# Kernel tuning notes

Hardware: AMD Instinct MI355X
Metric: run time of the kernel (lower is better)

Reference implementation:

```python
import jax, jax.numpy as jnp
import numpy as np

# dims: batch, seq, model dim, heads, head_k_dim, head_v_dim, conv size
B, S, D, H, DK, DV, K = 1, 2048, 1024, 8, 128, 128, 4
KD, VD = H * DK, H * DV  # key_dim, value_dim


def _silu(x):
    return x * jax.nn.sigmoid(x)


def _l2norm(x, eps=1e-6):
    return x * jax.lax.rsqrt(jnp.sum(x * x, -1, keepdims=True) + eps)


def _causal_conv_silu(x, w):
    # depthwise causal conv1d (ShortConvolution, activation='silu', no bias)
    # x: [b, s, d], w: [d, K]
    Kc = w.shape[1]
    xp = jnp.pad(x, ((0, 0), (Kc - 1, 0), (0, 0)))
    y = sum(xp[:, i:i + x.shape[1], :] * w[:, i] for i in range(Kc))
    return _silu(y)


def _rmsnorm(x, w, eps=1e-5):
    return x * jax.lax.rsqrt(jnp.mean(x * x, -1, keepdims=True) + eps) * w


def _kda(q, k, v, g, beta):
    # gated delta-rule linear attention (KDA), recurrent form == chunk_kda math
    # q,k,g: [B,S,H,DK]; v: [B,S,H,DV]; beta: [B,S,H]
    scale = DK ** -0.5
    qn = _l2norm(q) * scale  # use_qk_l2norm_in_kernel=True
    kn = _l2norm(k)

    def step(Sm, inp):
        q_t, k_t, v_t, g_t, b_t = inp  # [B,H,DK], [B,H,DK], [B,H,DV], [B,H,DK], [B,H]
        Sm = Sm * jnp.exp(g_t)[..., None]                    # per-key-channel decay
        v_new = (v_t - jnp.einsum('bhk,bhkv->bhv', k_t, Sm)) * b_t[..., None]
        Sm = Sm + k_t[..., None] * v_new[..., None, :]       # delta-rule update
        o_t = jnp.einsum('bhk,bhkv->bhv', q_t, Sm)
        return Sm, o_t

    xs = (jnp.swapaxes(qn, 0, 1), jnp.swapaxes(kn, 0, 1), jnp.swapaxes(v, 0, 1),
          jnp.swapaxes(g, 0, 1), jnp.swapaxes(beta, 0, 1))
    S0 = jnp.zeros((q.shape[0], H, DK, DV), jnp.float32)
    _, o = jax.lax.scan(step, S0, xs)
    return jnp.swapaxes(o, 0, 1)  # [B,S,H,DV]


def setup_inputs() -> dict:
    key = jax.random.key(0)
    ks = jax.random.split(key, 20)

    def w(k, shape, fan_in):
        return jax.random.normal(k, shape, jnp.float32) / np.sqrt(fan_in)

    return {
        'x': jax.random.normal(ks[0], (B, S, D), jnp.float32),
        've': jax.random.normal(ks[1], (B, S, D), jnp.float32),
        'sa_lambdas': jax.random.uniform(ks[2], (2,), jnp.float32),
        'Wq': w(ks[3], (KD, D), D), 'Wk': w(ks[4], (KD, D), D), 'Wv': w(ks[5], (VD, D), D),
        'Wo': w(ks[6], (D, VD), VD),
        'wq_conv': w(ks[7], (KD, K), K), 'wk_conv': w(ks[8], (KD, K), K), 'wv_conv': w(ks[9], (VD, K), K),
        'Wf1': w(ks[10], (DV, D), D), 'Wf2': w(ks[11], (KD, DV), DV),
        'Wb': w(ks[12], (H, D), D),
        'A_log': jnp.log(jax.random.uniform(ks[13], (H,), jnp.float32, 1.0, 16.0)),
        'dt_bias': jnp.zeros((KD,), jnp.float32),
        'Wg1': w(ks[14], (DV, D), D), 'Wg2': w(ks[15], (VD, DV), DV),
        'bg2': jnp.zeros((VD,), jnp.float32),
        'w_norm': jnp.ones((DV,), jnp.float32),
    }


def reference(x, ve, sa_lambdas, Wq, Wk, Wv, Wo, wq_conv, wk_conv, wv_conv,
              Wf1, Wf2, Wb, A_log, dt_bias, Wg1, Wg2, bg2, w_norm):
    b, s, _ = x.shape
    # q/k/v projections + short causal conv with silu
    q = _causal_conv_silu(x @ Wq.T, wq_conv)
    k = _causal_conv_silu(x @ Wk.T, wk_conv)
    v = _causal_conv_silu(x @ Wv.T, wv_conv)
    # fused_kda_gate: g = -exp(A_log) * softplus(f_proj(x) + dt_bias), per [H, DK]
    g = (x @ Wf1.T) @ Wf2.T
    g = jax.nn.softplus((g + dt_bias).astype(jnp.float32)).reshape(b, s, H, DK)
    g = -jnp.exp(A_log)[None, None, :, None] * g
    beta = jax.nn.sigmoid((x @ Wb.T).astype(jnp.float32))  # [b,s,H]
    q = q.reshape(b, s, H, DK)
    k = k.reshape(b, s, H, DK)
    v = v.reshape(b, s, H, DV)
    # mix v with value-embedding ve (3-D branch of _mix_v_with_ve)
    ve_v = _causal_conv_silu(ve @ Wv.T, wv_conv).reshape(b, s, H, DV)
    v = sa_lambdas[0] * v + sa_lambdas[1] * ve_v
    o = _kda(q, k, v, g, beta)  # [b,s,H,DV]
    # FusedRMSNormGated(activation='sigmoid'): rmsnorm(o)*w then gate
    g_out = ((x @ Wg1.T) @ Wg2.T + bg2).reshape(b, s, H, DV)
    o = _rmsnorm(o, w_norm) * jax.nn.sigmoid(g_out)
    return o.reshape(b, s, VD) @ Wo.T
```

## Files before the change

### kernel.cpp

```cpp
#include <hip/hip_runtime.h>
#include <math.h>
#include <stdint.h>

#define S_LEN 2048
#define DMODEL 1024
#define NH 8
#define DK_ 128
#define DV_ 128
#define KD_ 1024
#define KCONV 4
#define CW 32
#define NW2 64
#define PREB_STRIDE 17408
#define TKH_OFF 0
#define QHT_OFF 4096
#define KCT_OFF 8192
#define TV_OFF 12288
#define NN_OFF 16384
#define RS 164
#define GS 20

typedef short bf16x8 __attribute__((ext_vector_type(8)));
typedef float f32x4 __attribute__((ext_vector_type(4)));

__device__ __forceinline__ uint16_t f2bf(float f) {
  uint32_t u = __float_as_uint(f);
  u += 0x7FFF + ((u >> 16) & 1);
  return (uint16_t)(u >> 16);
}
__device__ __forceinline__ float bf2f(uint16_t u) {
  return __uint_as_float((uint32_t)u << 16);
}
__device__ __forceinline__ void glds16(const uint16_t* g, uint16_t* l) {
  __builtin_amdgcn_global_load_lds(
      (const __attribute__((address_space(1))) void*)g,
      (__attribute__((address_space(3))) void*)l, 16, 0, 0);
}
__device__ __forceinline__ float dot4(float4 a, float4 b) {
  return fmaf(a.w, b.w, fmaf(a.z, b.z, fmaf(a.y, b.y, a.x * b.x)));
}
__device__ __forceinline__ float4 f4add(float4 a, float4 b) {
  float4 r; r.x = a.x + b.x; r.y = a.y + b.y; r.z = a.z + b.z; r.w = a.w + b.w; return r;
}
__device__ __forceinline__ float4 f4sub(float4 a, float4 b) {
  float4 r; r.x = a.x - b.x; r.y = a.y - b.y; r.z = a.z - b.z; r.w = a.w - b.w; return r;
}
__device__ __forceinline__ float4 f4mul(float4 a, float4 b) {
  float4 r; r.x = a.x * b.x; r.y = a.y * b.y; r.z = a.z * b.z; r.w = a.w * b.w; return r;
}
__device__ __forceinline__ float4 f4s(float4 a, float s) {
  float4 r; r.x = a.x * s; r.y = a.y * s; r.z = a.z * s; r.w = a.w * s; return r;
}
__device__ __forceinline__ float4 f4expc(float4 a) {
  float4 r;
  r.x = expf(fminf(a.x, 0.f)); r.y = expf(fminf(a.y, 0.f));
  r.z = expf(fminf(a.z, 0.f)); r.w = expf(fminf(a.w, 0.f));
  return r;
}
__device__ __forceinline__ float4 f4exp(float4 a) {
  float4 r; r.x = expf(a.x); r.y = expf(a.y); r.z = expf(a.z); r.w = expf(a.w); return r;
}
__device__ __forceinline__ uint4 pack8(float4 a, float4 b) {
  uint4 r;
  r.x = (uint32_t)f2bf(a.x) | ((uint32_t)f2bf(a.y) << 16);
  r.y = (uint32_t)f2bf(a.z) | ((uint32_t)f2bf(a.w) << 16);
  r.z = (uint32_t)f2bf(b.x) | ((uint32_t)f2bf(b.y) << 16);
  r.w = (uint32_t)f2bf(b.z) | ((uint32_t)f2bf(b.w) << 16);
  return r;
}
__device__ __forceinline__ uint2 pack4(f32x4 a) {
  uint2 r;
  r.x = (uint32_t)f2bf(a[0]) | ((uint32_t)f2bf(a[1]) << 16);
  r.y = (uint32_t)f2bf(a[2]) | ((uint32_t)f2bf(a[3]) << 16);
  return r;
}
union U4B8 { uint4 u; bf16x8 b; };
__device__ __forceinline__ bf16x8 u2b(uint4 u) { U4B8 x; x.u = u; return x.b; }

#define DPPADD(x, ctrl) \
  x += __int_as_float(__builtin_amdgcn_update_dpp(0, __float_as_int(x), ctrl, 0xF, 0xF, true))

__device__ __forceinline__ void row8_sum2(float& a, float& b) {
  DPPADD(a, 0xB1); DPPADD(b, 0xB1);
  DPPADD(a, 0x4E); DPPADD(b, 0x4E);
  DPPADD(a, 0x141); DPPADD(b, 0x141);
}
__device__ __forceinline__ void row8_arr8x2(float* x, float* y) {
#pragma unroll
  for (int i = 0; i < 8; i++) { DPPADD(x[i], 0xB1); DPPADD(y[i], 0xB1); }
#pragma unroll
  for (int i = 0; i < 8; i++) { DPPADD(x[i], 0x4E); DPPADD(y[i], 0x4E); }
#pragma unroll
  for (int i = 0; i < 8; i++) { DPPADD(x[i], 0x141); DPPADD(y[i], 0x141); }
}

struct CastArgs {
  const float* s[8];
  uint16_t* d[8];
  int n[8];
};
__global__ __launch_bounds__(256) void cast_multi(CastArgs a, const float* __restrict__ Wb,
                                                  uint16_t* __restrict__ Wbp) {
  int i = blockIdx.y;
  if (i == 8) {
    for (int idx = blockIdx.x * 256 + threadIdx.x; idx < 128 * 1024; idx += 256 * 256) {
      int r = idx >> 10;
      Wbp[idx] = (r < 8) ? f2bf(Wb[idx]) : (uint16_t)0;
    }
    return;
  }
  const int step = gridDim.x * 256 * 8;
  for (int base = (blockIdx.x * 256 + threadIdx.x) * 8; base < a.n[i]; base += step) {
    const float4* sp = (const float4*)(a.s[i] + base);
    float4 x0 = sp[0], x1 = sp[1];
    *(uint4*)(a.d[i] + base) = pack8(x0, x1);
  }
}

__global__ __launch_bounds__(256) void gemm_wc(
    const float* __restrict__ A,
    const float* __restrict__ B,
    uint16_t* __restrict__ C) {
  __shared__ float As[16][68];
  __shared__ float Bs[16][68];
  const int tid = threadIdx.x;
  const int m0 = blockIdx.y * 64, n0 = blockIdx.x * 64;
  const int tx = tid & 15, ty = tid >> 4;
  const int lk = tid & 15, lr = tid >> 4;
  const int bc = tid & 63, bkr = tid >> 6;
  float acc[4][4] = {};
  for (int k0 = 0; k0 < 128; k0 += 16) {
#pragma unroll
    for (int i = 0; i < 4; i++) {
      As[lk][lr + 16 * i] = A[(size_t)(m0 + lr + 16 * i) * 128 + k0 + lk];
      Bs[bkr + 4 * i][bc] = B[(size_t)(k0 + bkr + 4 * i) * 1024 + n0 + bc];
    }
    __syncthreads();
#pragma unroll
    for (int kk = 0; kk < 16; kk++) {
      float4 a4 = *(const float4*)&As[kk][ty * 4];
      float4 b4 = *(const float4*)&Bs[kk][tx * 4];
      float av[4] = {a4.x, a4.y, a4.z, a4.w};
      float bv[4] = {b4.x, b4.y, b4.z, b4.w};
#pragma unroll
      for (int i = 0; i < 4; i++)
#pragma unroll
        for (int jx = 0; jx < 4; jx++) acc[i][jx] = fmaf(av[i], bv[jx], acc[i][jx]);
    }
    __syncthreads();
  }
#pragma unroll
  for (int i = 0; i < 4; i++)
#pragma unroll
    for (int jx = 0; jx < 4; jx++)
      C[(size_t)(m0 + ty * 4 + i) * 1024 + n0 + tx * 4 + jx] = f2bf(acc[i][jx]);
}

__device__ __forceinline__ void gemm_body(
    const uint16_t* __restrict__ A, const uint16_t* __restrict__ B, void* C,
    int N, int K, int outbf, int bx, int by, int tid,
    uint16_t* Asb, uint16_t* Bsb) {
  const int n0 = bx * 128;
  if (n0 >= N) return;
  const int w = tid >> 6, lane = tid & 63;
  const int m0 = by * 128;
  const int mw = (w & 1) * 64, nw = (w >> 1) * 64;
  const int c0 = tid, c1 = 256 + tid;
  const int r0 = c0 >> 2, cl0 = (c0 & 3) ^ ((r0 >> 2) & 3);
  const int r1 = c1 >> 2, cl1 = (c1 & 3) ^ ((r1 >> 2) & 3);
  const uint16_t* gA0 = A + (size_t)(m0 + r0) * K + cl0 * 8;
  const uint16_t* gA1 = A + (size_t)(m0 + r1) * K + cl1 * 8;
  const uint16_t* gB0 = B + (size_t)(n0 + r0) * K + cl0 * 8;
  const uint16_t* gB1 = B + (size_t)(n0 + r1) * K + cl1 * 8;
  uint16_t* lA0 = Asb + w * 512;
  uint16_t* lA1 = Asb + 2048 + w * 512;
  uint16_t* lB0 = Bsb + w * 512;
  uint16_t* lB1 = Bsb + 2048 + w * 512;

  const int l15 = lane & 15, q = lane >> 4;
  const int ccq = q ^ ((l15 >> 2) & 3);

  f32x4 acc[4][4] = {};
  for (int k0 = 0; k0 < K; k0 += 32) {
    glds16(gA0 + k0, lA0);
    glds16(gA1 + k0, lA1);
    glds16(gB0 + k0, lB0);
    glds16(gB1 + k0, lB1);
    __syncthreads();
    bf16x8 af[4], bfr[4];
#pragma unroll
    for (int i = 0; i < 4; i++)
      af[i] = *(const bf16x8*)&Asb[(mw + i * 16 + l15) * 32 + ccq * 8];
#pragma unroll
    for (int jx = 0; jx < 4; jx++)
      bfr[jx] = *(const bf16x8*)&Bsb[(nw + jx * 16 + l15) * 32 + ccq * 8];
#pragma unroll
    for (int i = 0; i < 4; i++)
#pragma unroll
      for (int jx = 0; jx < 4; jx++)
        acc[i][jx] = __builtin_amdgcn_mfma_f32_16x16x32_bf16(af[i], bfr[jx],
                                                             acc[i][jx], 0, 0, 0);
    __syncthreads();
  }
#pragma unroll
  for (int i = 0; i < 4; i++) {
#pragma unroll
    for (int jx = 0; jx < 4; jx++) {
      int n = n0 + nw + jx * 16 + l15;
#pragma unroll
      for (int r = 0; r < 4; r++) {
        int m = m0 + mw + i * 16 + q * 4 + r;
        if (outbf)
          ((uint16_t*)C)[(size_t)m * N + n] = f2bf(acc[i][jx][r]);
        else
          ((float*)C)[(size_t)m * N + n] = acc[i][jx][r];
      }
    }
  }
}

struct GJobs {
  const uint16_t* A[8];
  const uint16_t* B[8];
  void* C[8];
  int N[8];
  int outbf[8];
};
__global__ __launch_bounds__(256) void gemm_mfma(GJobs j, int K) {
  __shared__ uint16_t Asb[128 * 32];
  __shared__ uint16_t Bsb[128 * 32];
  const int z = blockIdx.z;
  gemm_body(j.A[z], j.B[z], j.C[z], j.N[z], K, j.outbf[z],
            blockIdx.x, blockIdx.y, threadIdx.x, Asb, Bsb);
}

__global__ __launch_bounds__(256) void conv_silu_mix(
    const uint16_t* __restrict__ qp, const uint16_t* __restrict__ kp,
    const uint16_t* __restrict__ vp, const uint16_t* __restrict__ vep,
    const float* __restrict__ wq, const float* __restrict__ wk,
    const float* __restrict__ wv, const float* __restrict__ lam,
    float* __restrict__ qc, float* __restrict__ kc, float* __restrict__ vmx) {
  int idx = blockIdx.x * 256 + threadIdx.x;
  if (idx >= S_LEN * KD_ / 8) return;
  int s = idx >> 7;
  int d0 = (idx & 127) * 8;
  const float lam0 = lam[0], lam1 = lam[1];

  union { uint4 u; ushort h[8]; } t;
  size_t base = (size_t)s * KD_ + d0;

  {
    float4 w4[8];
#pragma unroll
    for (int c = 0; c < 8; c++) w4[c] = *(const float4*)(wq + (size_t)d0 * 4 + c * 4);
    float acc[8] = {};
#pragma unroll
    for (int i = 0; i < KCONV; i++) {
      int ss = s - (KCONV - 1) + i;
      if (ss < 0) continue;
      t.u = *(const uint4*)(qp + (size_t)ss * KD_ + d0);
      float wi[8] = {w4[0].x, w4[1].x, w4[2].x, w4[3].x, w4[4].x, w4[5].x, w4[6].x, w4[7].x};
      if (i == 1) { for (int c = 0; c < 8; c++) wi[c] = ((const float*)&w4[c])[1]; }
      if (i == 2) { for (int c = 0; c < 8; c++) wi[c] = ((const float*)&w4[c])[2]; }
      if (i == 3) { for (int c = 0; c < 8; c++) wi[c] = ((const float*)&w4[c])[3]; }
#pragma unroll
      for (int c = 0; c < 8; c++) acc[c] = fmaf(bf2f(t.h[c]), wi[c], acc[c]);
    }
    float out[8];
#pragma unroll
    for (int c = 0; c < 8; c++) out[c] = acc[c] / (1.f + expf(-acc[c]));
    *(float4*)(qc + base) = *(float4*)&out[0];
    *(float4*)(qc + base + 4) = *(float4*)&out[4];
  }
  {
    float4 w4[8];
#pragma unroll
    for (int c = 0; c < 8; c++) w4[c] = *(const float4*)(wk + (size_t)d0 * 4 + c * 4);
    float acc[8] = {};
#pragma unroll
    for (int i = 0; i < KCONV; i++) {
      int ss = s - (KCONV - 1) + i;
      if (ss < 0) continue;
      t.u = *(const uint4*)(kp + (size_t)ss * KD_ + d0);
#pragma unroll
      for (int c = 0; c < 8; c++)
        acc[c] = fmaf(bf2f(t.h[c]), ((const float*)&w4[c])[i], acc[c]);
    }
    float out[8];
#pragma unroll
    for (int c = 0; c < 8; c++) out[c] = acc[c] / (1.f + expf(-acc[c]));
    *(float4*)(kc + base) = *(float4*)&out[0];
    *(float4*)(kc + base + 4) = *(float4*)&out[4];
  }
  {
    float4 w4[8];
#pragma unroll
    for (int c = 0; c < 8; c++) w4[c] = *(const float4*)(wv + (size_t)d0 * 4 + c * 4);
    float av[8] = {}, ae[8] = {};
#pragma unroll
    for (int i = 0; i < KCONV; i++) {
      int ss = s - (KCONV - 1) + i;
      if (ss < 0) continue;
      size_t off = (size_t)ss * KD_ + d0;
      t.u = *(const uint4*)(vp + off);
#pragma unroll
      for (int c = 0; c < 8; c++)
        av[c] = fmaf(bf2f(t.h[c]), ((const float*)&w4[c])[i], av[c]);
      t.u = *(const uint4*)(vep + off);
#pragma unroll
      for (int c = 0; c < 8; c++)
        ae[c] = fmaf(bf2f(t.h[c]), ((const float*)&w4[c])[i], ae[c]);
    }
    float out[8];
#pragma unroll
    for (int c = 0; c < 8; c++) {
      float sv = av[c] / (1.f + expf(-av[c]));
      float se = ae[c] / (1.f + expf(-ae[c]));
      out[c] = lam0 * sv + lam1 * se;
    }
    *(float4*)(vmx + base) = *(float4*)&out[0];
    *(float4*)(vmx + base + 4) = *(float4*)&out[4];
  }
}

__global__ __launch_bounds__(256) void kda_pre(
    const float* __restrict__ qc, const float* __restrict__ kc,
    const float* __restrict__ graw, const float* __restrict__ vm,
    const float* __restrict__ bpre, const float* __restrict__ dt_bias,
    const float* __restrict__ A_log, uint16_t* __restrict__ preB,
    float* __restrict__ preF) {
  __shared__ float kls[32 * RS];
  __shared__ float Gls[32 * RS];
  __shared__ float Mcm[32 * 36];
  __shared__ float bls[32];
  const int w = blockIdx.x >> 3, h = blockIdx.x & 7;
  const int tid = threadIdx.x;
  const int t = tid >> 3, kq = tid & 7;
  const int wv = tid >> 6;
  const size_t gb = (size_t)blockIdx.x * PREB_STRIDE;
  const size_t gf = (size_t)blockIdx.x * 128;

  size_t roff = (size_t)(w * CW + t) * KD_ + h * DK_ + kq * 16;
  float4 kv[4], qv[4], gv[4], dtb[4];
#pragma unroll
  for (int i = 0; i < 4; i++) {
    kv[i] = *(const float4*)(kc + roff + i * 4);
    qv[i] = *(const float4*)(qc + roff + i * 4);
    gv[i] = *(const float4*)(graw + roff + i * 4);
    dtb[i] = *(const float4*)(dt_bias + h * DK_ + kq * 16 + i * 4);
  }
  const float Ahead = expf(A_log[h]);
  if (tid < 32) {
    float b = bpre[(size_t)(w * CW + tid) * 128 + h];
    bls[tid] = 1.f / (1.f + expf(-b));
  }
  float src[32];
  if (tid >= 128) {
    int c2 = tid - 128;
#pragma unroll
    for (int t2 = 0; t2 < 32; t2++)
      src[t2] = vm[(size_t)(w * CW + t2) * KD_ + h * DV_ + c2];
  }
#pragma unroll
  for (int i = 0; i < 4; i++) {
    float vsp[4];
    float xin[4] = {gv[i].x + dtb[i].x, gv[i].y + dtb[i].y,
                    gv[i].z + dtb[i].z, gv[i].w + dtb[i].w};
#pragma unroll
    for (int e = 0; e < 4; e++)
      vsp[e] = (xin[e] > 20.f) ? xin[e] : log1pf(expf(xin[e]));
    gv[i].x = -Ahead * vsp[0]; gv[i].y = -Ahead * vsp[1];
    gv[i].z = -Ahead * vsp[2]; gv[i].w = -Ahead * vsp[3];
  }
  float sk = 0.f, sq = 0.f;
#pragma unroll
  for (int i = 0; i < 4; i++) {
    sk += dot4(kv[i], kv[i]);
    sq += dot4(qv[i], qv[i]);
  }
  row8_sum2(sk, sq);
  float rkn = rsqrtf(sk + 1e-6f);
  float rqn = rsqrtf(sq + 1e-6f) * 0.08838834764831845f;
#pragma unroll
  for (int i = 0; i < 4; i++) {
    kv[i] = f4s(kv[i], rkn);
    qv[i] = f4s(qv[i], rqn);
    *(float4*)&kls[t * RS + kq * GS + i * 4] = kv[i];
    *(float4*)&Gls[t * RS + kq * GS + i * 4] = gv[i];
  }
  __syncthreads();
  float4 Ga[4] = {};
#pragma unroll
  for (int jb = 0; jb < 4; jb++) {
    if (jb <= wv) {
#pragma unroll
      for (int jj = 0; jj < 8; jj++) {
        int j = jb * 8 + jj;
        bool inc = (jb < wv) || (j <= t);
#pragma unroll
        for (int i = 0; i < 4; i++) {
          float4 gj = *(const float4*)&Gls[j * RS + kq * GS + i * 4];
          if (inc) Ga[i] = f4add(Ga[i], gj);
        }
      }
    }
  }
  __syncthreads();
  float4 khr[4];
  float4 Pa[4];
#pragma unroll
  for (int i = 0; i < 4; i++) {
    *(float4*)&Gls[t * RS + kq * GS + i * 4] = Ga[i];
    Pa[i] = f4exp(Ga[i]);
    khr[i] = f4mul(kv[i], Pa[i]);
  }
  {
    float4 q0 = f4mul(qv[0], Pa[0]), q1 = f4mul(qv[1], Pa[1]);
    float4 q2 = f4mul(qv[2], Pa[2]), q3 = f4mul(qv[3], Pa[3]);
    *(uint4*)(preB + gb + QHT_OFF + t * 128 + kq * 16) = pack8(q0, q1);
    *(uint4*)(preB + gb + QHT_OFF + t * 128 + kq * 16 + 8) = pack8(q2, q3);
  }
  if (t == 31) {
#pragma unroll
    for (int i = 0; i < 4; i++)
      *(float4*)(preF + gf + kq * 16 + i * 4) = Pa[i];
  }
  __syncthreads();
#pragma unroll
  for (int i = 0; i < 4; i++) {
    float4 Gfi = *(const float4*)&Gls[31 * RS + kq * GS + i * 4];
    float4 ea = f4expc(f4sub(Gfi, Ga[i]));
    float4 kc4 = f4mul(kv[i], ea);
    float kk[4] = {kc4.x, kc4.y, kc4.z, kc4.w};
#pragma unroll
    for (int e = 0; e < 4; e++)
      preB[gb + KCT_OFF + (kq * 16 + i * 4 + e) * 32 + t] = f2bf(kk[e]);
  }
#pragma unroll
  for (int jb = 0; jb < 4; jb++) {
    if (jb <= wv) {
      float mp8[8], np8[8];
#pragma unroll
      for (int jj = 0; jj < 8; jj++) {
        int j = jb * 8 + jj;
        float m = 0.f, n = 0.f;
#pragma unroll
        for (int i = 0; i < 4; i++) {
          float4 kj = *(const float4*)&kls[j * RS + kq * GS + i * 4];
          float4 Gj = *(const float4*)&Gls[j * RS + kq * GS + i * 4];
          float4 e = f4expc(f4sub(Ga[i], Gj));
          float4 p = f4mul(kj, e);
          m += dot4(kv[i], p);
          n += dot4(qv[i], p);
        }
        mp8[jj] = (j < t) ? m : 0.f;
        np8[jj] = (j <= t) ? n : 0.f;
      }
      row8_arr8x2(mp8, np8);
#pragma unroll
      for (int jj = 0; jj < 8; jj++) {
        if (kq == jj) {
          int j = jb * 8 + jj;
          Mcm[j * 36 + t] = bls[t] * mp8[jj];
          preB[gb + NN_OFF + t * 32 + j] = f2bf(np8[jj]);
        }
      }
    } else {
      preB[gb + NN_OFF + t * 32 + jb * 8 + kq] = 0;
    }
  }
  float bl[32];
#pragma unroll
  for (int i = 0; i < 8; i++) {
    float4 b4 = *(const float4*)&bls[i * 4];
    bl[i * 4 + 0] = b4.x; bl[i * 4 + 1] = b4.y;
    bl[i * 4 + 2] = b4.z; bl[i * 4 + 3] = b4.w;
  }
  __syncthreads();
#pragma unroll
  for (int i = 0; i < 4; i++)
    *(float4*)&kls[t * RS + kq * GS + i * 4] = khr[i];
  __syncthreads();
  if (tid < 128) {
#pragma unroll
    for (int t2 = 0; t2 < 32; t2++)
      src[t2] = kls[t2 * RS + (tid >> 4) * GS + (tid & 15)];
  }
  const int c = tid;
  float acc[32];
#pragma unroll
  for (int i = 0; i < 32; i++) acc[i] = 0.f;
#pragma unroll
  for (int t2 = 0; t2 < 32; t2++) {
    float val = fmaf(bl[t2], src[t2], -acc[t2]);
    if (c < 128)
      preB[gb + TKH_OFF + t2 * 128 + c] = f2bf(val);
    else
      preB[gb + TV_OFF + t2 * 128 + (c - 128)] = f2bf(val);
#pragma unroll
    for (int t3 = t2 + 1; t3 < 32; t3++)
      acc[t3] = fmaf(Mcm[t2 * 36 + t3], val, acc[t3]);
  }
}

__global__ __launch_bounds__(256) void kda_scan_g2(
    const uint16_t* __restrict__ preB, const float* __restrict__ preF,
    float* __restrict__ o, const uint16_t* __restrict__ g1b,
    const uint16_t* __restrict__ Wg2b, float* __restrict__ g2raw) {
  __shared__ uint16_t tkh[2][32 * 136];
  __shared__ uint16_t qht[2][32 * 136];
  __shared__ uint16_t sbf[16 * 136];
  __shared__ uint16_t vbf[16 * 40];
  __shared__ uint16_t Asb[128 * 32];
  __shared__ uint16_t Bsb[128 * 32];
  const int bid = blockIdx.x;
  const int tid = threadIdx.x;

  if (bid >= 64) {
    int b2 = bid - 64;
    gemm_body(g1b, Wg2b, g2raw, 1024, 128, 0, b2 & 7, b2 >> 3, tid, Asb, Bsb);
    return;
  }

  const int h = bid & 7, cg = bid >> 3;
  const int wv = tid >> 6, lane = tid & 63;
  const int q = lane >> 4, l15 = lane & 15;

  auto stage = [&](int w, int buf) {
    size_t gbs = (size_t)(w * 8 + h) * PREB_STRIDE;
    const uint4* gt = (const uint4*)(preB + gbs + TKH_OFF);
    const uint4* gq = (const uint4*)(preB + gbs + QHT_OFF);
    int row = lane >> 1, half = lane & 1;
    uint4 a[8], b[8];
#pragma unroll
    for (int i = 0; i < 8; i++) {
      a[i] = gt[lane * 8 + i];
      b[i] = gq[lane * 8 + i];
    }
#pragma unroll
    for (int i = 0; i < 8; i++) {
      *(uint4*)&tkh[buf][row * 136 + half * 64 + i * 8] = a[i];
      *(uint4*)&qht[buf][row * 136 + half * 64 + i * 8] = b[i];
    }
  };

  f32x4 s[8] = {};

  if (wv == 1) stage(0, 0);
  __syncthreads();

  for (int w = 0; w < NW2; w++) {
    if (wv == 1) {
      if (w + 1 < NW2) stage(w + 1, (w + 1) & 1);
    } else if (wv == 0) {
      const int buf = w & 1;
      const size_t gbs = (size_t)(w * 8 + h) * PREB_STRIDE;
      uint4 kct[8], nrg[2];
      float4 pb[8];
      float tvv[2][4];
#pragma unroll
      for (int ki = 0; ki < 8; ki++)
        kct[ki] = *(const uint4*)(preB + gbs + KCT_OFF + (16 * ki + l15) * 32 + q * 8);
#pragma unroll
      for (int tt = 0; tt < 2; tt++)
        nrg[tt] = *(const uint4*)(preB + gbs + NN_OFF + (tt * 16 + l15) * 32 + q * 8);
#pragma unroll
      for (int ki = 0; ki < 8; ki++)
        pb[ki] = *(const float4*)(preF + (size_t)(w * 8 + h) * 128 + 16 * ki + q * 4);
#pragma unroll
      for (int tt = 0; tt < 2; tt++)
#pragma unroll
        for (int r = 0; r < 4; r++)
          tvv[tt][r] = bf2f(preB[gbs + TV_OFF + (tt * 16 + q * 4 + r) * 128 + cg * 16 + l15]);
#pragma unroll
      for (int ki = 0; ki < 8; ki++)
        *(uint2*)&sbf[l15 * 136 + 16 * ki + q * 4] = pack4(s[ki]);
      f32x4 aat[2] = {}, bbt[2] = {};
#pragma unroll
      for (int kc = 0; kc < 4; kc++) {
        bf16x8 bS = *(const bf16x8*)&sbf[l15 * 136 + kc * 32 + q * 8];
#pragma unroll
        for (int tt = 0; tt < 2; tt++) {
          bf16x8 aT = *(const bf16x8*)&tkh[buf][(tt * 16 + l15) * 136 + kc * 32 + q * 8];
          bf16x8 aQ = *(const bf16x8*)&qht[buf][(tt * 16 + l15) * 136 + kc * 32 + q * 8];
          aat[tt] = __builtin_amdgcn_mfma_f32_16x16x32_bf16(aT, bS, aat[tt], 0, 0, 0);
          bbt[tt] = __builtin_amdgcn_mfma_f32_16x16x32_bf16(aQ, bS, bbt[tt], 0, 0, 0);
        }
      }
#pragma unroll
      for (int tt = 0; tt < 2; tt++) {
        f32x4 vn;
#pragma unroll
        for (int r = 0; r < 4; r++) vn[r] = tvv[tt][r] - aat[tt][r];
        *(uint2*)&vbf[l15 * 40 + tt * 16 + q * 4] = pack4(vn);
      }
      bf16x8 bV = *(const bf16x8*)&vbf[l15 * 40 + q * 8];
#pragma unroll
      for (int tt = 0; tt < 2; tt++) {
        f32x4 ot = __builtin_amdgcn_mfma_f32_16x16x32_bf16(u2b(nrg[tt]), bV,
                                                           bbt[tt], 0, 0, 0);
#pragma unroll
        for (int r = 0; r < 4; r++)
          o[(size_t)(w * CW + tt * 16 + q * 4 + r) * KD_ + h * DK_ + cg * 16 + l15] = ot[r];
      }
#pragma unroll
      for (int ki = 0; ki < 8; ki++) {
#pragma unroll
        for (int r = 0; r < 4; r++) s[ki][r] *= pb[ki][r];
        s[ki] = __builtin_amdgcn_mfma_f32_16x16x32_bf16(u2b(kct[ki]), bV, s[ki], 0, 0, 0);
      }
    }
    __syncthreads();
  }
}

__global__ __launch_bounds__(64) void gated_rmsnorm(
    const float* __restrict__ o, const float* __restrict__ g2raw,
    const float* __restrict__ bg2, const float* __restrict__ wn,
    uint16_t* __restrict__ ob) {
  size_t base = (size_t)blockIdx.x * DV_;
  int t = threadIdx.x;
  float a = o[base + t], b = o[base + t + 64];
  float ss = a * a + b * b;
#pragma unroll
  for (int off = 32; off > 0; off >>= 1) ss += __shfl_xor(ss, off);
  float r = rsqrtf(ss * (1.f / 128.f) + 1e-5f);
  int c0 = (int)((base + t) & 1023), c1 = (int)((base + t + 64) & 1023);
  float ga = 1.f / (1.f + expf(-(g2raw[base + t] + bg2[c0])));
  float gb = 1.f / (1.f + expf(-(g2raw[base + t + 64] + bg2[c1])));
  ob[base + t] = f2bf(a * r * wn[t] * ga);
  ob[base + t + 64] = f2bf(b * r * wn[t + 64] * gb);
}

extern "C" void kernel_launch(void* const* d_in, const int* in_sizes, int n_in,
                              void* d_out, int out_size, void* d_ws, size_t ws_size,
                              hipStream_t stream) {
  const float* x = (const float*)d_in[0];
  const float* ve = (const float*)d_in[1];
  const float* lam = (const float*)d_in[2];
  const float* Wq = (const float*)d_in[3];
  const float* Wk = (const float*)d_in[4];
  const float* Wv = (const float*)d_in[5];
  const float* Wo = (const float*)d_in[6];
  const float* wq_conv = (const float*)d_in[7];
  const float* wk_conv = (const float*)d_in[8];
  const float* wv_conv = (const float*)d_in[9];
  const float* Wf1 = (const float*)d_in[10];
  const float* Wf2 = (const float*)d_in[11];
  const float* Wb = (const float*)d_in[12];
  const float* A_log = (const float*)d_in[13];
  const float* dt_bias = (const float*)d_in[14];
  const float* Wg1 = (const float*)d_in[15];
  const float* Wg2 = (const float*)d_in[16];
  const float* bg2 = (const float*)d_in[17];
  const float* w_norm = (const float*)d_in[18];
  float* out = (float*)d_out;

  float* ws = (float*)d_ws;
  const size_t SZ = (size_t)S_LEN * KD_;
  uint16_t* qpb = (uint16_t*)ws;
  uint16_t* kpb = (uint16_t*)(ws + SZ / 2);
  uint16_t* vpb = (uint16_t*)(ws + SZ);
  uint16_t* vepb = (uint16_t*)(ws + 3 * SZ / 2);
  float* q_c = ws + 2 * SZ;
  float* k_c = ws + 3 * SZ;
  float* v_mix = ws + 4 * SZ;
  float* graw = ws + 5 * SZ;
  float* o_buf = graw;
  float* g2raw = k_c;
  uint16_t* bws = (uint16_t*)(ws + 6 * SZ);
  uint16_t* xb = bws;
  uint16_t* veb = xb + SZ;
  uint16_t* Wqb = veb + SZ;
  uint16_t* Wkb = Wqb + (size_t)KD_ * DMODEL;
  uint16_t* Wvb = Wkb + (size_t)KD_ * DMODEL;
  uint16_t* Wob = Wvb + (size_t)KD_ * DMODEL;
  uint16_t* Wg1b = Wob + (size_t)DMODEL * KD_;
  uint16_t* Wg2b = Wg1b + (size_t)DV_ * DMODEL;
  uint16_t* Wcb = Wg2b + (size_t)KD_ * DV_;
  uint16_t* Wbp = Wcb + (size_t)KD_ * DMODEL;
  uint16_t* g1b = Wbp + (size_t)128 * 1024;
  uint16_t* ob = g1b + (size_t)S_LEN * DV_;
  float* bpre2 = ws + 18 * (size_t)1024 * 1024;
  float* preF = ws + (size_t)20 * 1024 * 1024;
  uint16_t* preB = (uint16_t*)(ws + (size_t)20 * 1024 * 1024 + 65536 + 64);

  dim3 blk(256);

  CastArgs ca;
  ca.s[0] = x;   ca.d[0] = xb;   ca.n[0] = S_LEN * DMODEL;
  ca.s[1] = ve;  ca.d[1] = veb;  ca.n[1] = S_LEN * DMODEL;
  ca.s[2] = Wq;  ca.d[2] = Wqb;  ca.n[2] = KD_ * DMODEL;
  ca.s[3] = Wk;  ca.d[3] = Wkb;  ca.n[3] = KD_ * DMODEL;
  ca.s[4] = Wv;  ca.d[4] = Wvb;  ca.n[4] = KD_ * DMODEL;
  ca.s[5] = Wo;  ca.d[5] = Wob;  ca.n[5] = DMODEL * KD_;
  ca.s[6] = Wg1; ca.d[6] = Wg1b; ca.n[6] = DV_ * DMODEL;
  ca.s[7] = Wg2; ca.d[7] = Wg2b; ca.n[7] = KD_ * DV_;
  cast_multi<<<dim3(256, 9), blk, 0, stream>>>(ca, Wb, Wbp);

  gemm_wc<<<dim3(16, 16), blk, 0, stream>>>(Wf2, Wf1, Wcb);

  GJobs jq;
  jq.A[0] = xb;  jq.B[0] = Wqb;  jq.C[0] = qpb;   jq.N[0] = KD_; jq.outbf[0] = 1;
  jq.A[1] = xb;  jq.B[1] = Wkb;  jq.C[1] = kpb;   jq.N[1] = KD_; jq.outbf[1] = 1;
  jq.A[2] = xb;  jq.B[2] = Wvb;  jq.C[2] = vpb;   jq.N[2] = KD_; jq.outbf[2] = 1;
  jq.A[3] = veb; jq.B[3] = Wvb;  jq.C[3] = vepb;  jq.N[3] = KD_; jq.outbf[3] = 1;
  jq.A[4] = xb;  jq.B[4] = Wg1b; jq.C[4] = g1b;   jq.N[4] = DV_; jq.outbf[4] = 1;
  jq.A[5] = xb;  jq.B[5] = Wcb;  jq.C[5] = graw;  jq.N[5] = KD_; jq.outbf[5] = 0;
  jq.A[6] = xb;  jq.B[6] = Wbp;  jq.C[6] = bpre2; jq.N[6] = 128; jq.outbf[6] = 0;
  gemm_mfma<<<dim3(8, 16, 7), blk, 0, stream>>>(jq, DMODEL);

  int conv_blocks = (S_LEN * KD_ / 8 + 255) / 256;
  conv_silu_mix<<<conv_blocks, blk, 0, stream>>>(qpb, kpb, vpb, vepb,
                                                 wq_conv, wk_conv, wv_conv, lam,
                                                 q_c, k_c, v_mix);

  kda_pre<<<dim3(NW2 * 8), blk, 0, stream>>>(q_c, k_c, graw, v_mix, bpre2,
                                             dt_bias, A_log, preB, preF);

  kda_scan_g2<<<dim3(192), blk, 0, stream>>>(preB, preF, o_buf, g1b, Wg2b, g2raw);

  gated_rmsnorm<<<dim3(S_LEN * NH), dim3(64), 0, stream>>>(o_buf, g2raw, bg2,
                                                           w_norm, ob);

  GJobs jo;
  jo.A[0] = ob; jo.B[0] = Wob; jo.C[0] = out; jo.N[0] = DMODEL; jo.outbf[0] = 0;
  gemm_mfma<<<dim3(8, 16, 1), blk, 0, stream>>>(jo, KD_);
}
```

Before: 384.9 us.

## Fuse KDA preprocessing into scan kernel with per-chunk flag handoff

```diff
diff --git a/kernel.cpp b/kernel.cpp
--- a/kernel.cpp
+++ b/kernel.cpp
@@ -100,10 +100,13 @@
   int n[8];
 };
 __global__ __launch_bounds__(256) void cast_multi(CastArgs a, const float* __restrict__ Wb,
-                                                  uint16_t* __restrict__ Wbp) {
+                                                  uint16_t* __restrict__ Wbp,
+                                                  uint32_t* __restrict__ flags) {
   int i = blockIdx.y;
   if (i == 8) {
-    for (int idx = blockIdx.x * 256 + threadIdx.x; idx < 128 * 1024; idx += 256 * 256) {
+    int idx0 = blockIdx.x * 256 + threadIdx.x;
+    if (idx0 < NW2 * 8) flags[idx0] = 0;
+    for (int idx = idx0; idx < 128 * 1024; idx += 256 * 256) {
       int r = idx >> 10;
       Wbp[idx] = (r < 8) ? f2bf(Wb[idx]) : (uint16_t)0;
     }
@@ -259,12 +262,9 @@
       int ss = s - (KCONV - 1) + i;
       if (ss < 0) continue;
       t.u = *(const uint4*)(qp + (size_t)ss * KD_ + d0);
-      float wi[8] = {w4[0].x, w4[1].x, w4[2].x, w4[3].x, w4[4].x, w4[5].x, w4[6].x, w4[7].x};
-      if (i == 1) { for (int c = 0; c < 8; c++) wi[c] = ((const float*)&w4[c])[1]; }
-      if (i == 2) { for (int c = 0; c < 8; c++) wi[c] = ((const float*)&w4[c])[2]; }
-      if (i == 3) { for (int c = 0; c < 8; c++) wi[c] = ((const float*)&w4[c])[3]; }
-#pragma unroll
-      for (int c = 0; c < 8; c++) acc[c] = fmaf(bf2f(t.h[c]), wi[c], acc[c]);
+#pragma unroll
+      for (int c = 0; c < 8; c++)
+        acc[c] = fmaf(bf2f(t.h[c]), ((const float*)&w4[c])[i], acc[c]);
     }
     float out[8];
 #pragma unroll
@@ -323,22 +323,21 @@
   }
 }
 
-__global__ __launch_bounds__(256) void kda_pre(
+__device__ void kda_pre_body(
     const float* __restrict__ qc, const float* __restrict__ kc,
     const float* __restrict__ graw, const float* __restrict__ vm,
     const float* __restrict__ bpre, const float* __restrict__ dt_bias,
     const float* __restrict__ A_log, uint16_t* __restrict__ preB,
-    float* __restrict__ preF) {
-  __shared__ float kls[32 * RS];
-  __shared__ float Gls[32 * RS];
-  __shared__ float Mcm[32 * 36];
-  __shared__ float bls[32];
-  const int w = blockIdx.x >> 3, h = blockIdx.x & 7;
-  const int tid = threadIdx.x;
+    float* __restrict__ preF, uint32_t* __restrict__ flags,
+    int w, int h, int tid, unsigned char* smem) {
+  float* kls = (float*)smem;
+  float* Gls = (float*)(smem + 20992);
+  float* Mcm = (float*)(smem + 41984);
+  float* bls = (float*)(smem + 46592);
   const int t = tid >> 3, kq = tid & 7;
   const int wv = tid >> 6;
-  const size_t gb = (size_t)blockIdx.x * PREB_STRIDE;
-  const size_t gf = (size_t)blockIdx.x * 128;
+  const size_t gb = (size_t)(w * 8 + h) * PREB_STRIDE;
+  const size_t gf = (size_t)(w * 8 + h) * 128;
 
   size_t roff = (size_t)(w * CW + t) * KD_ + h * DK_ + kq * 16;
   float4 kv[4], qv[4], gv[4], dtb[4];
@@ -501,35 +500,60 @@
     for (int t3 = t2 + 1; t3 < 32; t3++)
       acc[t3] = fmaf(Mcm[t2 * 36 + t3], val, acc[t3]);
   }
-}
-
-__global__ __launch_bounds__(256) void kda_scan_g2(
-    const uint16_t* __restrict__ preB, const float* __restrict__ preF,
+  __threadfence();
+  __syncthreads();
+  if (tid == 0)
+    __hip_atomic_store(&flags[w * 8 + h], 1u, __ATOMIC_RELEASE,
+                       __HIP_MEMORY_SCOPE_AGENT);
+}
+
+__global__ __launch_bounds__(256) void kda_fused(
+    const uint16_t* __restrict__ preB_c, const float* __restrict__ preF_c,
     float* __restrict__ o, const uint16_t* __restrict__ g1b,
-    const uint16_t* __restrict__ Wg2b, float* __restrict__ g2raw) {
-  __shared__ uint16_t tkh[2][32 * 136];
-  __shared__ uint16_t qht[2][32 * 136];
-  __shared__ uint16_t sbf[16 * 136];
-  __shared__ uint16_t vbf[16 * 40];
-  __shared__ uint16_t Asb[128 * 32];
-  __shared__ uint16_t Bsb[128 * 32];
+    const uint16_t* __restrict__ Wg2b, float* __restrict__ g2raw,
+    const float* __restrict__ qc, const float* __restrict__ kc,
+    const float* __restrict__ graw, const float* __restrict__ vm,
+    const float* __restrict__ bpre, const float* __restrict__ dt_bias,
+    const float* __restrict__ A_log, uint16_t* __restrict__ preB,
+    float* __restrict__ preF, uint32_t* __restrict__ flags) {
+  __shared__ __align__(16) unsigned char smem[46720];
   const int bid = blockIdx.x;
   const int tid = threadIdx.x;
 
+  if (bid >= 192) {
+    const int pb = bid - 192;
+    const int h = pb & 7, wslot = pb >> 3;
+    for (int it = 0; it < 4; ++it)
+      kda_pre_body(qc, kc, graw, vm, bpre, dt_bias, A_log, preB, preF, flags,
+                   wslot + 16 * it, h, tid, smem);
+    return;
+  }
   if (bid >= 64) {
+    uint16_t* Asb = (uint16_t*)smem;
+    uint16_t* Bsb = (uint16_t*)(smem + 8192);
     int b2 = bid - 64;
     gemm_body(g1b, Wg2b, g2raw, 1024, 128, 0, b2 & 7, b2 >> 3, tid, Asb, Bsb);
     return;
   }
 
+  uint16_t* tkh = (uint16_t*)smem;
+  uint16_t* qht = (uint16_t*)(smem + 17408);
+  uint16_t* sbf = (uint16_t*)(smem + 34816);
+  uint16_t* vbf = (uint16_t*)(smem + 39168);
   const int h = bid & 7, cg = bid >> 3;
   const int wv = tid >> 6, lane = tid & 63;
   const int q = lane >> 4, l15 = lane & 15;
 
+  auto waitw = [&](int wi) {
+    while (__hip_atomic_load(&flags[wi * 8 + h], __ATOMIC_ACQUIRE,
+                             __HIP_MEMORY_SCOPE_AGENT) == 0u)
+      __builtin_amdgcn_s_sleep(2);
+  };
+
   auto stage = [&](int w, int buf) {
     size_t gbs = (size_t)(w * 8 + h) * PREB_STRIDE;
-    const uint4* gt = (const uint4*)(preB + gbs + TKH_OFF);
-    const uint4* gq = (const uint4*)(preB + gbs + QHT_OFF);
+    const uint4* gt = (const uint4*)(preB_c + gbs + TKH_OFF);
+    const uint4* gq = (const uint4*)(preB_c + gbs + QHT_OFF);
     int row = lane >> 1, half = lane & 1;
     uint4 a[8], b[8];
 #pragma unroll
@@ -539,20 +563,21 @@
     }
 #pragma unroll
     for (int i = 0; i < 8; i++) {
-      *(uint4*)&tkh[buf][row * 136 + half * 64 + i * 8] = a[i];
-      *(uint4*)&qht[buf][row * 136 + half * 64 + i * 8] = b[i];
+      *(uint4*)&tkh[buf * 4352 + row * 136 + half * 64 + i * 8] = a[i];
+      *(uint4*)&qht[buf * 4352 + row * 136 + half * 64 + i * 8] = b[i];
     }
   };
 
   f32x4 s[8] = {};
 
-  if (wv == 1) stage(0, 0);
+  if (wv == 1) { waitw(0); stage(0, 0); }
   __syncthreads();
 
   for (int w = 0; w < NW2; w++) {
     if (wv == 1) {
-      if (w + 1 < NW2) stage(w + 1, (w + 1) & 1);
+      if (w + 1 < NW2) { waitw(w + 1); stage(w + 1, (w + 1) & 1); }
     } else if (wv == 0) {
+      waitw(w);
       const int buf = w & 1;
       const size_t gbs = (size_t)(w * 8 + h) * PREB_STRIDE;
       uint4 kct[8], nrg[2];
@@ -560,29 +585,29 @@
       float tvv[2][4];
 #pragma unroll
       for (int ki = 0; ki < 8; ki++)
-        kct[ki] = *(const uint4*)(preB + gbs + KCT_OFF + (16 * ki + l15) * 32 + q * 8);
+        kct[ki] = *(const uint4*)(preB_c + gbs + KCT_OFF + (16 * ki + l15) * 32 + q * 8);
 #pragma unroll
       for (int tt = 0; tt < 2; tt++)
-        nrg[tt] = *(const uint4*)(preB + gbs + NN_OFF + (tt * 16 + l15) * 32 + q * 8);
+        nrg[tt] = *(const uint4*)(preB_c + gbs + NN_OFF + (tt * 16 + l15) * 32 + q * 8);
 #pragma unroll
       for (int ki = 0; ki < 8; ki++)
-        pb[ki] = *(const float4*)(preF + (size_t)(w * 8 + h) * 128 + 16 * ki + q * 4);
+        pb[ki] = *(const float4*)(preF_c + (size_t)(w * 8 + h) * 128 + 16 * ki + q * 4);
 #pragma unroll
       for (int tt = 0; tt < 2; tt++)
 #pragma unroll
         for (int r = 0; r < 4; r++)
-          tvv[tt][r] = bf2f(preB[gbs + TV_OFF + (tt * 16 + q * 4 + r) * 128 + cg * 16 + l15]);
+          tvv[tt][r] = bf2f(preB_c[gbs + TV_OFF + (tt * 16 + q * 4 + r) * 128 + cg * 16 + l15]);
 #pragma unroll
       for (int ki = 0; ki < 8; ki++)
         *(uint2*)&sbf[l15 * 136 + 16 * ki + q * 4] = pack4(s[ki]);
       f32x4 aat[2] = {}, bbt[2] = {};
 #pragma unroll
-      for (int kc = 0; kc < 4; kc++) {
-        bf16x8 bS = *(const bf16x8*)&sbf[l15 * 136 + kc * 32 + q * 8];
+      for (int kc2 = 0; kc2 < 4; kc2++) {
+        bf16x8 bS = *(const bf16x8*)&sbf[l15 * 136 + kc2 * 32 + q * 8];
 #pragma unroll
         for (int tt = 0; tt < 2; tt++) {
-          bf16x8 aT = *(const bf16x8*)&tkh[buf][(tt * 16 + l15) * 136 + kc * 32 + q * 8];
-          bf16x8 aQ = *(const bf16x8*)&qht[buf][(tt * 16 + l15) * 136 + kc * 32 + q * 8];
+          bf16x8 aT = *(const bf16x8*)&tkh[buf * 4352 + (tt * 16 + l15) * 136 + kc2 * 32 + q * 8];
+          bf16x8 aQ = *(const bf16x8*)&qht[buf * 4352 + (tt * 16 + l15) * 136 + kc2 * 32 + q * 8];
           aat[tt] = __builtin_amdgcn_mfma_f32_16x16x32_bf16(aT, bS, aat[tt], 0, 0, 0);
           bbt[tt] = __builtin_amdgcn_mfma_f32_16x16x32_bf16(aQ, bS, bbt[tt], 0, 0, 0);
         }
@@ -667,10 +692,10 @@
   float* v_mix = ws + 4 * SZ;
   float* graw = ws + 5 * SZ;
   float* o_buf = graw;
-  float* g2raw = k_c;
   uint16_t* bws = (uint16_t*)(ws + 6 * SZ);
   uint16_t* xb = bws;
   uint16_t* veb = xb + SZ;
+  float* g2raw = (float*)bws;
   uint16_t* Wqb = veb + SZ;
   uint16_t* Wkb = Wqb + (size_t)KD_ * DMODEL;
   uint16_t* Wvb = Wkb + (size_t)KD_ * DMODEL;
@@ -682,6 +707,7 @@
   uint16_t* g1b = Wbp + (size_t)128 * 1024;
   uint16_t* ob = g1b + (size_t)S_LEN * DV_;
   float* bpre2 = ws + 18 * (size_t)1024 * 1024;
+  uint32_t* flags = (uint32_t*)(ws + 19 * (size_t)1024 * 1024);
   float* preF = ws + (size_t)20 * 1024 * 1024;
   uint16_t* preB = (uint16_t*)(ws + (size_t)20 * 1024 * 1024 + 65536 + 64);
 
@@ -696,7 +722,7 @@
   ca.s[5] = Wo;  ca.d[5] = Wob;  ca.n[5] = DMODEL * KD_;
   ca.s[6] = Wg1; ca.d[6] = Wg1b; ca.n[6] = DV_ * DMODEL;
   ca.s[7] = Wg2; ca.d[7] = Wg2b; ca.n[7] = KD_ * DV_;
-  cast_multi<<<dim3(256, 9), blk, 0, stream>>>(ca, Wb, Wbp);
+  cast_multi<<<dim3(256, 9), blk, 0, stream>>>(ca, Wb, Wbp, flags);
 
   gemm_wc<<<dim3(16, 16), blk, 0, stream>>>(Wf2, Wf1, Wcb);
 
@@ -715,10 +741,9 @@
                                                  wq_conv, wk_conv, wv_conv, lam,
                                                  q_c, k_c, v_mix);
 
-  kda_pre<<<dim3(NW2 * 8), blk, 0, stream>>>(q_c, k_c, graw, v_mix, bpre2,
-                                             dt_bias, A_log, preB, preF);
-
-  kda_scan_g2<<<dim3(192), blk, 0, stream>>>(preB, preF, o_buf, g1b, Wg2b, g2raw);
+  kda_fused<<<dim3(320), blk, 0, stream>>>(preB, preF, o_buf, g1b, Wg2b, g2raw,
+                                           q_c, k_c, graw, v_mix, bpre2,
+                                           dt_bias, A_log, preB, preF, flags);
 
   gated_rmsnorm<<<dim3(S_LEN * NH), dim3(64), 0, stream>>>(o_buf, g2raw, bg2,
                                                            w_norm, ob);
```

Result: slower. 526.4 us (+36.8%).

## Fuse causal conv, SiLU and value mix into kda_pre kernel

Applied to the files above, without the earlier changes.

```diff
diff --git a/kernel.cpp b/kernel.cpp
--- a/kernel.cpp
+++ b/kernel.cpp
@@ -234,98 +234,12 @@
             blockIdx.x, blockIdx.y, threadIdx.x, Asb, Bsb);
 }
 
-__global__ __launch_bounds__(256) void conv_silu_mix(
-    const uint16_t* __restrict__ qp, const uint16_t* __restrict__ kp,
-    const uint16_t* __restrict__ vp, const uint16_t* __restrict__ vep,
+__global__ __launch_bounds__(256) void kda_pre(
+    const uint16_t* __restrict__ qpb, const uint16_t* __restrict__ kpb,
+    const uint16_t* __restrict__ vpb, const uint16_t* __restrict__ vepb,
     const float* __restrict__ wq, const float* __restrict__ wk,
     const float* __restrict__ wv, const float* __restrict__ lam,
-    float* __restrict__ qc, float* __restrict__ kc, float* __restrict__ vmx) {
-  int idx = blockIdx.x * 256 + threadIdx.x;
-  if (idx >= S_LEN * KD_ / 8) return;
-  int s = idx >> 7;
-  int d0 = (idx & 127) * 8;
-  const float lam0 = lam[0], lam1 = lam[1];
-
-  union { uint4 u; ushort h[8]; } t;
-  size_t base = (size_t)s * KD_ + d0;
-
-  {
-    float4 w4[8];
-#pragma unroll
-    for (int c = 0; c < 8; c++) w4[c] = *(const float4*)(wq + (size_t)d0 * 4 + c * 4);
-    float acc[8] = {};
-#pragma unroll
-    for (int i = 0; i < KCONV; i++) {
-      int ss = s - (KCONV - 1) + i;
-      if (ss < 0) continue;
-      t.u = *(const uint4*)(qp + (size_t)ss * KD_ + d0);
-      float wi[8] = {w4[0].x, w4[1].x, w4[2].x, w4[3].x, w4[4].x, w4[5].x, w4[6].x, w4[7].x};
-      if (i == 1) { for (int c = 0; c < 8; c++) wi[c] = ((const float*)&w4[c])[1]; }
-      if (i == 2) { for (int c = 0; c < 8; c++) wi[c] = ((const float*)&w4[c])[2]; }
-      if (i == 3) { for (int c = 0; c < 8; c++) wi[c] = ((const float*)&w4[c])[3]; }
-#pragma unroll
-      for (int c = 0; c < 8; c++) acc[c] = fmaf(bf2f(t.h[c]), wi[c], acc[c]);
-    }
-    float out[8];
-#pragma unroll
-    for (int c = 0; c < 8; c++) out[c] = acc[c] / (1.f + expf(-acc[c]));
-    *(float4*)(qc + base) = *(float4*)&out[0];
-    *(float4*)(qc + base + 4) = *(float4*)&out[4];
-  }
-  {
-    float4 w4[8];
-#pragma unroll
-    for (int c = 0; c < 8; c++) w4[c] = *(const float4*)(wk + (size_t)d0 * 4 + c * 4);
-    float acc[8] = {};
-#pragma unroll
-    for (int i = 0; i < KCONV; i++) {
-      int ss = s - (KCONV - 1) + i;
-      if (ss < 0) continue;
-      t.u = *(const uint4*)(kp + (size_t)ss * KD_ + d0);
-#pragma unroll
-      for (int c = 0; c < 8; c++)
-        acc[c] = fmaf(bf2f(t.h[c]), ((const float*)&w4[c])[i], acc[c]);
-    }
-    float out[8];
-#pragma unroll
-    for (int c = 0; c < 8; c++) out[c] = acc[c] / (1.f + expf(-acc[c]));
-    *(float4*)(kc + base) = *(float4*)&out[0];
-    *(float4*)(kc + base + 4) = *(float4*)&out[4];
-  }
-  {
-    float4 w4[8];
-#pragma unroll
-    for (int c = 0; c < 8; c++) w4[c] = *(const float4*)(wv + (size_t)d0 * 4 + c * 4);
-    float av[8] = {}, ae[8] = {};
-#pragma unroll
-    for (int i = 0; i < KCONV; i++) {
-      int ss = s - (KCONV - 1) + i;
-      if (ss < 0) continue;
-      size_t off = (size_t)ss * KD_ + d0;
-      t.u = *(const uint4*)(vp + off);
-#pragma unroll
-      for (int c = 0; c < 8; c++)
-        av[c] = fmaf(bf2f(t.h[c]), ((const float*)&w4[c])[i], av[c]);
-      t.u = *(const uint4*)(vep + off);
-#pragma unroll
-      for (int c = 0; c < 8; c++)
-        ae[c] = fmaf(bf2f(t.h[c]), ((const float*)&w4[c])[i], ae[c]);
-    }
-    float out[8];
-#pragma unroll
-    for (int c = 0; c < 8; c++) {
-      float sv = av[c] / (1.f + expf(-av[c]));
-      float se = ae[c] / (1.f + expf(-ae[c]));
-      out[c] = lam0 * sv + lam1 * se;
-    }
-    *(float4*)(vmx + base) = *(float4*)&out[0];
-    *(float4*)(vmx + base + 4) = *(float4*)&out[4];
-  }
-}
-
-__global__ __launch_bounds__(256) void kda_pre(
-    const float* __restrict__ qc, const float* __restrict__ kc,
-    const float* __restrict__ graw, const float* __restrict__ vm,
+    const float* __restrict__ graw,
     const float* __restrict__ bpre, const float* __restrict__ dt_bias,
     const float* __restrict__ A_log, uint16_t* __restrict__ preB,
     float* __restrict__ preF) {
@@ -336,31 +250,66 @@
   const int w = blockIdx.x >> 3, h = blockIdx.x & 7;
   const int tid = threadIdx.x;
   const int t = tid >> 3, kq = tid & 7;
-  const int wv = tid >> 6;
+  const int wv2 = tid >> 6;
   const size_t gb = (size_t)blockIdx.x * PREB_STRIDE;
   const size_t gf = (size_t)blockIdx.x * 128;
-
-  size_t roff = (size_t)(w * CW + t) * KD_ + h * DK_ + kq * 16;
-  float4 kv[4], qv[4], gv[4], dtb[4];
-#pragma unroll
-  for (int i = 0; i < 4; i++) {
-    kv[i] = *(const float4*)(kc + roff + i * 4);
-    qv[i] = *(const float4*)(qc + roff + i * 4);
+  const int row = w * CW + t;
+  const size_t d0 = (size_t)h * DK_ + kq * 16;
+
+  auto conv_silu8 = [&](const uint16_t* __restrict__ p, const float* __restrict__ wg,
+                        size_t db, float* out8) {
+    float4 w4[8];
+#pragma unroll
+    for (int c = 0; c < 8; c++) w4[c] = *(const float4*)(wg + (db + c) * 4);
+    float acc[8] = {};
+#pragma unroll
+    for (int i = 0; i < KCONV; i++) {
+      int ss = row - (KCONV - 1) + i;
+      if (ss < 0) continue;
+      union { uint4 u; ushort hx[8]; } t4;
+      t4.u = *(const uint4*)(p + (size_t)ss * KD_ + db);
+#pragma unroll
+      for (int c = 0; c < 8; c++)
+        acc[c] = fmaf(bf2f(t4.hx[c]), ((const float*)&w4[c])[i], acc[c]);
+    }
+#pragma unroll
+    for (int c = 0; c < 8; c++) out8[c] = acc[c] / (1.f + expf(-acc[c]));
+  };
+
+  float qv8[16], kv8[16], vv8[16], ve8[16];
+  conv_silu8(qpb, wq, d0, qv8);      conv_silu8(qpb, wq, d0 + 8, qv8 + 8);
+  conv_silu8(kpb, wk, d0, kv8);      conv_silu8(kpb, wk, d0 + 8, kv8 + 8);
+  conv_silu8(vpb, wv, d0, vv8);      conv_silu8(vpb, wv, d0 + 8, vv8 + 8);
+  conv_silu8(vepb, wv, d0, ve8);     conv_silu8(vepb, wv, d0 + 8, ve8 + 8);
+  const float lam0 = lam[0], lam1 = lam[1];
+  float4 vmix4[4];
+#pragma unroll
+  for (int i = 0; i < 4; i++) {
+    float m0v = lam0 * vv8[i * 4 + 0] + lam1 * ve8[i * 4 + 0];
+    float m1v = lam0 * vv8[i * 4 + 1] + lam1 * ve8[i * 4 + 1];
+    float m2v = lam0 * vv8[i * 4 + 2] + lam1 * ve8[i * 4 + 2];
+    float m3v = lam0 * vv8[i * 4 + 3] + lam1 * ve8[i * 4 + 3];
+    vmix4[i] = make_float4(m0v, m1v, m2v, m3v);
+  }
+  float4 kv[4], qv[4];
+#pragma unroll
+  for (int i = 0; i < 4; i++) {
+    kv[i] = make_float4(kv8[i * 4 + 0], kv8[i * 4 + 1], kv8[i * 4 + 2], kv8[i * 4 + 3]);
+    qv[i] = make_float4(qv8[i * 4 + 0], qv8[i * 4 + 1], qv8[i * 4 + 2], qv8[i * 4 + 3]);
+  }
+
+  float4 gv[4], dtb[4];
+  size_t roff = (size_t)row * KD_ + d0;
+#pragma unroll
+  for (int i = 0; i < 4; i++) {
     gv[i] = *(const float4*)(graw + roff + i * 4);
-    dtb[i] = *(const float4*)(dt_bias + h * DK_ + kq * 16 + i * 4);
+    dtb[i] = *(const float4*)(dt_bias + d0 + i * 4);
   }
   const float Ahead = expf(A_log[h]);
   if (tid < 32) {
     float b = bpre[(size_t)(w * CW + tid) * 128 + h];
     bls[tid] = 1.f / (1.f + expf(-b));
   }
-  float src[32];
-  if (tid >= 128) {
-    int c2 = tid - 128;
-#pragma unroll
-    for (int t2 = 0; t2 < 32; t2++)
-      src[t2] = vm[(size_t)(w * CW + t2) * KD_ + h * DV_ + c2];
-  }
 #pragma unroll
   for (int i = 0; i < 4; i++) {
     float vsp[4];
@@ -392,11 +341,11 @@
   float4 Ga[4] = {};
 #pragma unroll
   for (int jb = 0; jb < 4; jb++) {
-    if (jb <= wv) {
+    if (jb <= wv2) {
 #pragma unroll
       for (int jj = 0; jj < 8; jj++) {
         int j = jb * 8 + jj;
-        bool inc = (jb < wv) || (j <= t);
+        bool inc = (jb < wv2) || (j <= t);
 #pragma unroll
         for (int i = 0; i < 4; i++) {
           float4 gj = *(const float4*)&Gls[j * RS + kq * GS + i * 4];
@@ -438,7 +387,7 @@
   }
 #pragma unroll
   for (int jb = 0; jb < 4; jb++) {
-    if (jb <= wv) {
+    if (jb <= wv2) {
       float mp8[8], np8[8];
 #pragma unroll
       for (int jj = 0; jj < 8; jj++) {
@@ -478,13 +427,21 @@
   }
   __syncthreads();
 #pragma unroll
-  for (int i = 0; i < 4; i++)
+  for (int i = 0; i < 4; i++) {
     *(float4*)&kls[t * RS + kq * GS + i * 4] = khr[i];
+    *(float4*)&Gls[t * RS + kq * GS + i * 4] = vmix4[i];
+  }
   __syncthreads();
+  float src[32];
   if (tid < 128) {
 #pragma unroll
     for (int t2 = 0; t2 < 32; t2++)
       src[t2] = kls[t2 * RS + (tid >> 4) * GS + (tid & 15)];
+  } else {
+    int c2 = tid - 128;
+#pragma unroll
+    for (int t2 = 0; t2 < 32; t2++)
+      src[t2] = Gls[t2 * RS + (c2 >> 4) * GS + (c2 & 15)];
   }
   const int c = tid;
   float acc[32];
@@ -662,12 +619,9 @@
   uint16_t* kpb = (uint16_t*)(ws + SZ / 2);
   uint16_t* vpb = (uint16_t*)(ws + SZ);
   uint16_t* vepb = (uint16_t*)(ws + 3 * SZ / 2);
-  float* q_c = ws + 2 * SZ;
-  float* k_c = ws + 3 * SZ;
-  float* v_mix = ws + 4 * SZ;
+  float* g2raw = ws + 3 * SZ;
   float* graw = ws + 5 * SZ;
   float* o_buf = graw;
-  float* g2raw = k_c;
   uint16_t* bws = (uint16_t*)(ws + 6 * SZ);
   uint16_t* xb = bws;
   uint16_t* veb = xb + SZ;
@@ -710,13 +664,10 @@
   jq.A[6] = xb;  jq.B[6] = Wbp;  jq.C[6] = bpre2; jq.N[6] = 128; jq.outbf[6] = 0;
   gemm_mfma<<<dim3(8, 16, 7), blk, 0, stream>>>(jq, DMODEL);
 
-  int conv_blocks = (S_LEN * KD_ / 8 + 255) / 256;
-  conv_silu_mix<<<conv_blocks, blk, 0, stream>>>(qpb, kpb, vpb, vepb,
-                                                 wq_conv, wk_conv, wv_conv, lam,
-                                                 q_c, k_c, v_mix);
-
-  kda_pre<<<dim3(NW2 * 8), blk, 0, stream>>>(q_c, k_c, graw, v_mix, bpre2,
-                                             dt_bias, A_log, preB, preF);
+  kda_pre<<<dim3(NW2 * 8), blk, 0, stream>>>(qpb, kpb, vpb, vepb,
+                                             wq_conv, wk_conv, wv_conv, lam,
+                                             graw, bpre2, dt_bias, A_log,
+                                             preB, preF);
 
   kda_scan_g2<<<dim3(192), blk, 0, stream>>>(preB, preF, o_buf, g1b, Wg2b, g2raw);
 
```

Measured after the change: 414.9 us. 7.8% more time.
